# Performance work log

Hardware: AMD Instinct MI355X
Metric: run time of the kernel (lower is better)

The kernel has to match this reference:

```python
import math
import jax, jax.numpy as jnp
import numpy as np

N, D = 16384, 1024


def setup_inputs() -> dict:
    key = jax.random.key(0)
    k1, k2 = jax.random.split(key)
    return {
        "image_embeddings_aligned": jax.random.normal(k1, (N, D), dtype=jnp.float32),
        "text_embeddings_aligned": jax.random.normal(k2, (N, D), dtype=jnp.float32),
        "logit_scale": jnp.asarray(math.log(20.0), dtype=jnp.float32),  # stored as log(init)
        "logit_bias": jnp.asarray(-10.0, dtype=jnp.float32),
    }


def _l2_normalize(x, eps=1e-12):
    # matches F.normalize(p=2, dim=-1)
    n = jnp.linalg.norm(x, axis=-1, keepdims=True)
    return x / jnp.maximum(n, eps)


def reference(image_embeddings_aligned, text_embeddings_aligned, logit_scale, logit_bias):
    img = _l2_normalize(image_embeddings_aligned)
    txt = _l2_normalize(text_embeddings_aligned)
    # [N, N] pairwise logits
    logits = jnp.exp(logit_scale) * jnp.einsum("nd,md->nm", img, txt) + logit_bias
    n = logits.shape[0]
    labels = 2.0 * jnp.eye(n, dtype=logits.dtype) - 1.0  # +1 on diagonal, -1 off
    loss_matrix = jax.nn.log_sigmoid(labels * logits)
    siglip_loss = -jnp.mean(loss_matrix)  # total_loss (structure_lambda == 0)
    return siglip_loss
```

## Files before the change

kernel.cpp:

```cpp
#include <hip/hip_runtime.h>

#define NROWS 16384
#define DIM   1024
#define QSCALE 32.0f
#define E8M0S  0x7A7A7A7Au

typedef int    v4i    __attribute__((ext_vector_type(4)));
typedef int    v8i    __attribute__((ext_vector_type(8)));
typedef float  f32x16 __attribute__((ext_vector_type(16)));

__device__ __forceinline__ void glds16(const void* g, void* l) {
    __builtin_amdgcn_global_load_lds(
        (const __attribute__((address_space(1))) void*)g,
        (__attribute__((address_space(3))) void*)l,
        16, 0, 0);
}

__device__ __forceinline__ float fexp2(float x) {
#if __has_builtin(__builtin_amdgcn_exp2f)
    return __builtin_amdgcn_exp2f(x);
#else
    return exp2f(x);
#endif
}
__device__ __forceinline__ float flog2(float x) {
#if __has_builtin(__builtin_amdgcn_logf)
    return __builtin_amdgcn_logf(x);
#else
    return log2f(x);
#endif
}

__device__ __forceinline__ unsigned fp4_nib(float y) {
    unsigned s = (__float_as_uint(y) >> 31) << 3;
    float a = fminf(fabsf(y), 6.0f);
    unsigned c = (unsigned)(a >= 0.25f) + (unsigned)(a >= 0.75f) +
                 (unsigned)(a >= 1.25f) + (unsigned)(a >= 1.75f) +
                 (unsigned)(a >= 2.5f)  + (unsigned)(a >= 3.5f)  +
                 (unsigned)(a >= 5.0f);
    return c | s;
}

__global__ __launch_bounds__(256) void norm_fused(
    const float* __restrict__ img,
    const float* __restrict__ txt,
    unsigned char* __restrict__ imgQ,
    unsigned char* __restrict__ txtQ,
    const float* __restrict__ lscale,
    const float* __restrict__ lbias,
    float* __restrict__ diagPart) {
    const int t    = threadIdx.x;
    const int lane = t & 63;
    const int wave = t >> 6;
    const int gw   = blockIdx.x * 4 + wave;
    const float sc   = __expf(lscale[0]);
    const float bias = lbias[0];

    for (int row = gw; row < NROWS; row += 8192) {
        const float4* pi = (const float4*)(img + (size_t)row * DIM);
        const float4* pt = (const float4*)(txt + (size_t)row * DIM);
        float4 vi[4], vt[4];
        float ssi = 0.0f, sst = 0.0f, dot = 0.0f;
        #pragma unroll
        for (int j = 0; j < 4; ++j) {
            vi[j] = pi[lane + 64 * j];
            vt[j] = pt[lane + 64 * j];
            ssi += vi[j].x*vi[j].x + vi[j].y*vi[j].y + vi[j].z*vi[j].z + vi[j].w*vi[j].w;
            sst += vt[j].x*vt[j].x + vt[j].y*vt[j].y + vt[j].z*vt[j].z + vt[j].w*vt[j].w;
            dot += vi[j].x*vt[j].x + vi[j].y*vt[j].y + vi[j].z*vt[j].z + vi[j].w*vt[j].w;
        }
        #pragma unroll
        for (int off = 1; off < 64; off <<= 1) {
            ssi += __shfl_xor(ssi, off, 64);
            sst += __shfl_xor(sst, off, 64);
            dot += __shfl_xor(dot, off, 64);
        }
        const float ii = 1.0f / fmaxf(sqrtf(ssi), 1e-12f);
        const float it = 1.0f / fmaxf(sqrtf(sst), 1e-12f);
        if (lane == 0) diagPart[row] = -fmaf(sc, dot * ii * it, bias);

        const float qi = ii * QSCALE, qt = it * QSCALE;
        ushort* oi = (ushort*)(imgQ + (size_t)row * 512);
        ushort* ot = (ushort*)(txtQ + (size_t)row * 512);
        #pragma unroll
        for (int j = 0; j < 4; ++j) {
            unsigned p = fp4_nib(vi[j].x * qi)        | (fp4_nib(vi[j].y * qi) << 4) |
                         (fp4_nib(vi[j].z * qi) << 8) | (fp4_nib(vi[j].w * qi) << 12);
            unsigned q = fp4_nib(vt[j].x * qt)        | (fp4_nib(vt[j].y * qt) << 4) |
                         (fp4_nib(vt[j].z * qt) << 8) | (fp4_nib(vt[j].w * qt) << 12);
            oi[lane + 64 * j] = (ushort)p;
            ot[lane + 64 * j] = (ushort)q;
        }
    }
}

__global__ __launch_bounds__(512, 2) void siglip_gemm(
    const unsigned char* __restrict__ A,
    const unsigned char* __restrict__ B,
    const float* __restrict__ lscale,
    const float* __restrict__ lbias,
    float* __restrict__ gemmPart)
{
    __shared__ unsigned char sA[2][256 * 128];
    __shared__ unsigned char sB[2][256 * 128];
    __shared__ float wred[8];

    const int t    = threadIdx.x;
    const int lane = t & 63;
    const int wave = t >> 6;
    const int wr   = wave >> 2;
    const int wc   = wave & 3;
    const int r31  = lane & 31;
    const int h    = lane >> 5;
    const int xr   = (r31 & 7) ^ ((r31 >> 4) & 1);

    const int GRID_N = NROWS / 256;
    const int GM = 16;
    int b = blockIdx.x;
    int group = b / (GM * GRID_N);
    int ing   = b % (GM * GRID_N);
    int brow  = group * GM + (ing % GM);
    int bcol  = ing / GM;

    const size_t aBase = (size_t)brow * 256;
    const size_t bBase = (size_t)bcol * 256;

    const int srow = lane >> 3;
    const int c0   = (lane & 7) ^ srow;
    const int d01  = (c0 & 1) ? -16 : 16;

    const unsigned char* aP = A + (size_t)(aBase + wave * 32 + srow) * 512 + c0 * 16;
    const unsigned char* bP = B + (size_t)(bBase + wave * 32 + srow) * 512 + c0 * 16;

    int rbA[4], rbB[2];
    #pragma unroll
    for (int i = 0; i < 4; ++i) rbA[i] = (wr * 128 + i * 32 + r31) * 128;
    #pragma unroll
    for (int i = 0; i < 2; ++i) rbB[i] = (wc * 64 + i * 32 + r31) * 128;

    f32x16 acc[4][2] = {};

    {
        char* la = ((char*)sA[0]) + wave * 4096;
        char* lb = ((char*)sB[0]) + wave * 4096;
        #pragma unroll
        for (int j = 0; j < 4; ++j) {
            const int tog = ((j >> 1) & 1) ? d01 : 0;
            glds16(aP + j * 8 * 512 + tog, la + j * 1024);
            glds16(bP + j * 8 * 512 + tog, lb + j * 1024);
        }
    }
    __syncthreads();

    #pragma unroll
    for (int k = 0; k < 4; ++k) {
        const int cur = k & 1;

        v4i af[4][4], bf[4][2];
        #pragma unroll
        for (int ks = 0; ks < 4; ++ks) {
            const int s = ((ks * 2 + h) ^ xr) * 16;
            #pragma unroll
            for (int i = 0; i < 4; ++i)
                af[ks][i] = *(const v4i*)(sA[cur] + rbA[i] + s);
            #pragma unroll
            for (int n = 0; n < 2; ++n)
                bf[ks][n] = *(const v4i*)(sB[cur] + rbB[n] + s);
        }

        if (k < 3) {
            const unsigned char* aN = aP + (k + 1) * 128;
            const unsigned char* bN = bP + (k + 1) * 128;
            char* la = ((char*)sA[cur ^ 1]) + wave * 4096;
            char* lb = ((char*)sB[cur ^ 1]) + wave * 4096;
            #pragma unroll
            for (int j = 0; j < 4; ++j) {
                const int tog = ((j >> 1) & 1) ? d01 : 0;
                glds16(aN + j * 8 * 512 + tog, la + j * 1024);
                glds16(bN + j * 8 * 512 + tog, lb + j * 1024);
            }
        }

        #pragma unroll
        for (int ks = 0; ks < 4; ++ks) {
            #pragma unroll
            for (int mi = 0; mi < 4; ++mi) {
                v8i a8 = __builtin_shufflevector(af[ks][mi], af[ks][mi],
                                                 0, 1, 2, 3, -1, -1, -1, -1);
                #pragma unroll
                for (int ni = 0; ni < 2; ++ni) {
                    v8i b8 = __builtin_shufflevector(bf[ks][ni], bf[ks][ni],
                                                     0, 1, 2, 3, -1, -1, -1, -1);
                    acc[mi][ni] = __builtin_amdgcn_mfma_scale_f32_32x32x64_f8f6f4(
                        a8, b8, acc[mi][ni],
                        4, 4,
                        0, (int)E8M0S,
                        0, (int)E8M0S);
                }
            }
        }

        __syncthreads();
    }

    const float l2e   = 1.44269504088896341f;
    const float scale = __expf(lscale[0]);
    const float aCo   = scale * l2e;
    const float bCo   = lbias[0] * l2e;
    float local = 0.0f;
    #pragma unroll
    for (int mi = 0; mi < 4; ++mi)
        #pragma unroll
        for (int ni = 0; ni < 2; ++ni)
            #pragma unroll
            for (int r = 0; r < 16; r += 4) {
                float e0 = fexp2(fmaf(aCo, acc[mi][ni][r + 0], bCo));
                float e1 = fexp2(fmaf(aCo, acc[mi][ni][r + 1], bCo));
                float e2 = fexp2(fmaf(aCo, acc[mi][ni][r + 2], bCo));
                float e3 = fexp2(fmaf(aCo, acc[mi][ni][r + 3], bCo));
                float p  = ((1.0f + e0) * (1.0f + e1)) *
                           ((1.0f + e2) * (1.0f + e3));
                local += flog2(p);
            }

    #pragma unroll
    for (int off = 32; off > 0; off >>= 1) local += __shfl_down(local, off, 64);
    if (lane == 0) wred[wave] = local;
    __syncthreads();
    if (t == 0) {
        float tot = 0.0f;
        #pragma unroll
        for (int i = 0; i < 8; ++i) tot += wred[i];
        gemmPart[blockIdx.x] = tot * 0.69314718055994531f;
    }
}

__global__ __launch_bounds__(1024) void finalize_kernel(
    const float* __restrict__ parts, float* __restrict__ out) {
    __shared__ float wr[16];
    const int t    = threadIdx.x;
    const int lane = t & 63;
    const int wave = t >> 6;
    const float4* p4 = (const float4*)parts;
    float s = 0.0f;
    for (int i = t; i < 5120; i += 1024) {
        float4 v = p4[i];
        s += v.x + v.y + v.z + v.w;
    }
    #pragma unroll
    for (int off = 32; off > 0; off >>= 1) s += __shfl_down(s, off, 64);
    if (lane == 0) wr[wave] = s;
    __syncthreads();
    if (t == 0) {
        float tot = 0.0f;
        #pragma unroll
        for (int i = 0; i < 16; ++i) tot += wr[i];
        out[0] = tot / 268435456.0f;
    }
}

extern "C" void kernel_launch(void* const* d_in, const int* in_sizes, int n_in,
                              void* d_out, int out_size, void* d_ws, size_t ws_size,
                              hipStream_t stream) {
    const float* img    = (const float*)d_in[0];
    const float* txt    = (const float*)d_in[1];
    const float* lscale = (const float*)d_in[2];
    const float* lbias  = (const float*)d_in[3];
    float* out = (float*)d_out;

    char* ws = (char*)d_ws;
    unsigned char* imgQ = (unsigned char*)ws;
    unsigned char* txtQ = (unsigned char*)(ws + (size_t)NROWS * 512);
    float* parts   = (float*)(ws + (size_t)2 * NROWS * 512);
    float* diagPart = parts;
    float* gemmPart = parts + NROWS;

    norm_fused<<<2048, 256, 0, stream>>>(img, txt, imgQ, txtQ, lscale, lbias, diagPart);
    siglip_gemm<<<dim3((NROWS / 256) * (NROWS / 256)), 512, 0, stream>>>(
        imgQ, txtQ, lscale, lbias, gemmPart);
    finalize_kernel<<<1, 1024, 0, stream>>>(parts, out);
}
```

Before: 312.0 us.

## Remap blocks per XCD and interleave LDS reads with MFMA using fine-grained barriers

Block-to-tile mapping changes so each of the 8 XCDs handles a contiguous band of B columns, aiming for better L2 reuse. The main loop now waits on the prefetch with explicit vmcnt and s_barrier instead of __syncthreads. LDS fragment loads move into each ks step so they can alternate with MFMA groups, and s_setprio raises wave priority around the MFMAs. This lowers register pressure and overlaps LDS reads with matrix math, but adds many barriers per iteration and depends on hand-counted waitcnt values being correct.

```diff
diff --git a/kernel.cpp b/kernel.cpp
--- a/kernel.cpp
+++ b/kernel.cpp
@@ -114,13 +114,11 @@
     const int h    = lane >> 5;
     const int xr   = (r31 & 7) ^ ((r31 >> 4) & 1);
 
-    const int GRID_N = NROWS / 256;
-    const int GM = 16;
-    int b = blockIdx.x;
-    int group = b / (GM * GRID_N);
-    int ing   = b % (GM * GRID_N);
-    int brow  = group * GM + (ing % GM);
-    int bcol  = ing / GM;
+    const int b    = blockIdx.x;
+    const int xcd  = b & 7;
+    const int lb   = b >> 3;
+    const int bcol = xcd * 8 + (lb & 7);
+    const int brow = lb >> 3;
 
     const size_t aBase = (size_t)brow * 256;
     const size_t bBase = (size_t)bcol * 256;
@@ -142,54 +140,58 @@
 
     {
         char* la = ((char*)sA[0]) + wave * 4096;
-        char* lb = ((char*)sB[0]) + wave * 4096;
+        char* lb_ = ((char*)sB[0]) + wave * 4096;
         #pragma unroll
         for (int j = 0; j < 4; ++j) {
             const int tog = ((j >> 1) & 1) ? d01 : 0;
             glds16(aP + j * 8 * 512 + tog, la + j * 1024);
-            glds16(bP + j * 8 * 512 + tog, lb + j * 1024);
-        }
-    }
-    __syncthreads();
+            glds16(bP + j * 8 * 512 + tog, lb_ + j * 1024);
+        }
+    }
 
     #pragma unroll
     for (int k = 0; k < 4; ++k) {
         const int cur = k & 1;
-
-        v4i af[4][4], bf[4][2];
-        #pragma unroll
-        for (int ks = 0; ks < 4; ++ks) {
-            const int s = ((ks * 2 + h) ^ xr) * 16;
-            #pragma unroll
-            for (int i = 0; i < 4; ++i)
-                af[ks][i] = *(const v4i*)(sA[cur] + rbA[i] + s);
-            #pragma unroll
-            for (int n = 0; n < 2; ++n)
-                bf[ks][n] = *(const v4i*)(sB[cur] + rbB[n] + s);
-        }
 
         if (k < 3) {
             const unsigned char* aN = aP + (k + 1) * 128;
             const unsigned char* bN = bP + (k + 1) * 128;
             char* la = ((char*)sA[cur ^ 1]) + wave * 4096;
-            char* lb = ((char*)sB[cur ^ 1]) + wave * 4096;
+            char* lb_ = ((char*)sB[cur ^ 1]) + wave * 4096;
             #pragma unroll
             for (int j = 0; j < 4; ++j) {
                 const int tog = ((j >> 1) & 1) ? d01 : 0;
                 glds16(aN + j * 8 * 512 + tog, la + j * 1024);
-                glds16(bN + j * 8 * 512 + tog, lb + j * 1024);
+                glds16(bN + j * 8 * 512 + tog, lb_ + j * 1024);
             }
-        }
+            asm volatile("s_waitcnt vmcnt(8)" ::: "memory");
+        } else {
+            asm volatile("s_waitcnt vmcnt(0)" ::: "memory");
+        }
+        __builtin_amdgcn_s_barrier();
 
         #pragma unroll
         for (int ks = 0; ks < 4; ++ks) {
+            const int s = ((ks * 2 + h) ^ xr) * 16;
+            v4i av[4], bv[2];
+            #pragma unroll
+            for (int i = 0; i < 4; ++i)
+                av[i] = *(const v4i*)(sA[cur] + rbA[i] + s);
+            #pragma unroll
+            for (int n = 0; n < 2; ++n)
+                bv[n] = *(const v4i*)(sB[cur] + rbB[n] + s);
+
+            __builtin_amdgcn_s_barrier();
+            asm volatile("s_waitcnt lgkmcnt(0)" ::: "memory");
+            __builtin_amdgcn_sched_barrier(0);
+            __builtin_amdgcn_s_setprio(1);
             #pragma unroll
             for (int mi = 0; mi < 4; ++mi) {
-                v8i a8 = __builtin_shufflevector(af[ks][mi], af[ks][mi],
+                v8i a8 = __builtin_shufflevector(av[mi], av[mi],
                                                  0, 1, 2, 3, -1, -1, -1, -1);
                 #pragma unroll
                 for (int ni = 0; ni < 2; ++ni) {
-                    v8i b8 = __builtin_shufflevector(bf[ks][ni], bf[ks][ni],
+                    v8i b8 = __builtin_shufflevector(bv[ni], bv[ni],
                                                      0, 1, 2, 3, -1, -1, -1, -1);
                     acc[mi][ni] = __builtin_amdgcn_mfma_scale_f32_32x32x64_f8f6f4(
                         a8, b8, acc[mi][ni],
@@ -198,9 +200,9 @@
                         0, (int)E8M0S);
                 }
             }
-        }
-
-        __syncthreads();
+            __builtin_amdgcn_s_setprio(0);
+            __builtin_amdgcn_s_barrier();
+        }
     }
 
     const float l2e   = 1.44269504088896341f;
```

Result: slower. 329.8 us (+5.7%).
